# Kernel optimization log

Hardware: AMD Instinct MI355X
Metric: run time of the kernel (lower is better)

## Reference

```python
import jax, jax.numpy as jnp
import numpy as np

TAU_MEM = 20.0
TAU_SYN = 5.0
ALPHA_MEM = float(np.exp(-1.0 / TAU_MEM))
ALPHA_SYN = float(np.exp(-1.0 / TAU_SYN))
CONNECTIVITY = 0.1
SPECTRAL_RADIUS = 0.9


def setup_inputs() -> dict:
    key = jax.random.key(0)
    k1, k2, k3, k4 = jax.random.split(key, 4)
    B, D, N = 2048, 256, 512
    rates = jax.random.normal(k1, (B, D), dtype=jnp.float32)
    input_weight = jax.random.normal(k2, (N, D), dtype=jnp.float32) * 0.1
    W = jax.random.normal(k3, (N, N), dtype=jnp.float32)
    mask = (jax.random.uniform(k4, (N, N)) < CONNECTIVITY).astype(jnp.float32)
    W = W * mask
    # mirror torch init: scale by spectral_radius / max eigvalsh
    max_eig = jnp.linalg.eigvalsh(W)[-1]
    W = W * (SPECTRAL_RADIUS / max_eig)
    return {
        "rates": rates,
        "input_weight": input_weight,
        "reservoir_weight": W,
        "v_mem": jnp.zeros((B, N), dtype=jnp.float32),
        "current": jnp.zeros((B, N), dtype=jnp.float32),
        "n_steps": 64,
    }


def reference(rates, input_weight, reservoir_weight, v_mem, current, n_steps):
    dtype = rates.dtype
    # input current is identical every step in the original loop -> hoist it
    input_current = rates @ input_weight.T  # (B, N)

    def step(carry, _):
        v, c, spike_sum = carry
        rec = (c > 0).astype(dtype) @ reservoir_weight  # (B, N)
        c = ALPHA_SYN * c + (1.0 - ALPHA_SYN) * (input_current + rec)
        v = ALPHA_MEM * v + (1.0 - ALPHA_MEM) * c
        spike_sum = spike_sum + (v > 0).astype(dtype)
        return (v, c, spike_sum), None

    (v, c, spike_sum), _ = jax.lax.scan(
        step, (v_mem, current, jnp.zeros_like(v_mem)), None, length=n_steps
    )
    readout = spike_sum / n_steps  # == stack(spikes).mean(dim=1)
    return readout, (v, c)
```

## Files before the change

### kernel.cpp

```cpp
#include <hip/hip_runtime.h>
#include <stdint.h>


#define N_NEU 512
#define B_ROWS 2048
#define D_IN 256
#define R_PB 8
#define NBLK (B_ROWS / R_PB)

#define WS_PERM    0
#define WS_RANK    2048
#define WS_CNT     4096
#define WS_CNTW    8192
#define WS_IBASE   8256
#define WS_WBASE   8320
#define WS_IDX     16384
#define WS_WT      81920

#define SPK_OFF(k)  ((k) << 3)
#define SPK_BUF     4096

__global__ __launch_bounds__(256) void lsm_count(
    const float* __restrict__ W, uint32_t* __restrict__ ws)
{
    int t  = threadIdx.x;
    int k0 = blockIdx.x * 4;
    int c0 = 0, c1 = 0;
    #pragma unroll
    for (int kk = 0; kk < 4; ++kk) {
        const float* row = W + (size_t)(k0 + kk) * N_NEU;
        c0 += (row[t]       != 0.0f) ? 1 : 0;
        c1 += (row[t + 256] != 0.0f) ? 1 : 0;
    }
    if (c0) atomicAdd(&ws[(WS_CNT >> 2) + t],       (uint32_t)c0);
    if (c1) atomicAdd(&ws[(WS_CNT >> 2) + t + 256], (uint32_t)c1);
}

__global__ __launch_bounds__(512) void lsm_sort(uint32_t* __restrict__ ws)
{
    __shared__ int hist[N_NEU + 1];
    __shared__ int csort[N_NEU];
    __shared__ int gcw[8];

    int t = threadIdx.x;
    int creal = (int)ws[(WS_CNT >> 2) + t];
    for (int i = t; i < N_NEU + 1; i += 512) hist[i] = 0;
    __syncthreads();
    atomicAdd(&hist[creal], 1);
    __syncthreads();
    if (t == 0) {
        int acc = 0;
        for (int v = 0; v <= N_NEU; ++v) { int h = hist[v]; hist[v] = acc; acc += h; }
    }
    __syncthreads();
    int rank = atomicAdd(&hist[creal], 1);
    ws[(WS_PERM >> 2) + rank] = (uint32_t)t;
    ws[(WS_RANK >> 2) + t]    = (uint32_t)rank;
    csort[rank] = creal;
    __syncthreads();
    if (t < 8) {
        int cw = csort[t * 64 + 63];
        cw = (cw + 7) & ~7;
        gcw[t] = cw;
        ws[(WS_CNTW >> 2) + t] = (uint32_t)cw;
    }
    __syncthreads();
    if (t == 0) {
        int ai = 0, aw = 0;
        for (int g = 0; g < 8; ++g) {
            ws[(WS_IBASE >> 2) + g] = (uint32_t)ai;
            ws[(WS_WBASE >> 2) + g] = (uint32_t)aw;
            ai += gcw[g] * 64 * 2;
            aw += gcw[g] * 64 * 4;
        }
    }
    __syncthreads();
    int wg = rank >> 6, ls = rank & 63;
    int cw = gcw[wg];
    uint32_t ib = ws[(WS_IBASE >> 2) + wg];
    uint32_t wb = ws[(WS_WBASE >> 2) + wg];
    char* base = (char*)ws;
    for (int j = creal; j < cw; ++j) {
        *(unsigned short*)(base + WS_IDX + ib + (j >> 3) * 1024 + ls * 16 + (j & 7) * 2) = 0;
        *(float*)(base + WS_WT + wb + (j >> 3) * 2048 + ls * 32 + (j & 7) * 4) = 0.0f;
    }
}

__global__ __launch_bounds__(64) void lsm_fill(
    const float* __restrict__ W, uint32_t* __restrict__ ws)
{
    int c    = blockIdx.x;
    int lane = threadIdx.x;
    char* base = (char*)ws;
    uint32_t rank = ws[(WS_RANK >> 2) + c];
    int wg = (int)(rank >> 6), ls = (int)(rank & 63);
    uint32_t ib = ws[(WS_IBASE >> 2) + wg];
    uint32_t wb = ws[(WS_WBASE >> 2) + wg];

    __shared__ int ctr;
    if (lane == 0) ctr = 0;
    __syncthreads();

    for (int k = lane; k < N_NEU; k += 64) {
        float wv = W[(size_t)k * N_NEU + c];
        if (wv != 0.0f) {
            int j = atomicAdd(&ctr, 1);
            *(unsigned short*)(base + WS_IDX + ib + (j >> 3) * 1024 + ls * 16 + (j & 7) * 2)
                = (unsigned short)SPK_OFF(k);
            *(float*)(base + WS_WT + wb + (j >> 3) * 2048 + ls * 32 + (j & 7) * 4) = wv;
        }
    }
}

#define GATH(P, X, B) \
    P##0 = *(const uint2*)((B) + ((X).x & 0xffffu)); \
    P##1 = *(const uint2*)((B) + ((X).x >> 16));     \
    P##2 = *(const uint2*)((B) + ((X).y & 0xffffu)); \
    P##3 = *(const uint2*)((B) + ((X).y >> 16));     \
    P##4 = *(const uint2*)((B) + ((X).z & 0xffffu)); \
    P##5 = *(const uint2*)((B) + ((X).z >> 16));     \
    P##6 = *(const uint2*)((B) + ((X).w & 0xffffu)); \
    P##7 = *(const uint2*)((B) + ((X).w >> 16));

#define C1(S, W) \
    rec0 = fmaf((W), (float)((S).x & 0xffu),         rec0); \
    rec1 = fmaf((W), (float)(((S).x >> 8) & 0xffu),  rec1); \
    rec2 = fmaf((W), (float)(((S).x >> 16) & 0xffu), rec2); \
    rec3 = fmaf((W), (float)((S).x >> 24),           rec3); \
    rec4 = fmaf((W), (float)((S).y & 0xffu),         rec4); \
    rec5 = fmaf((W), (float)(((S).y >> 8) & 0xffu),  rec5); \
    rec6 = fmaf((W), (float)(((S).y >> 16) & 0xffu), rec6); \
    rec7 = fmaf((W), (float)((S).y >> 24),           rec7);

#define CONS(P, WA, WB) \
    C1(P##0, (WA).x) C1(P##1, (WA).y) C1(P##2, (WA).z) C1(P##3, (WA).w) \
    C1(P##4, (WB).x) C1(P##5, (WB).y) C1(P##6, (WB).z) C1(P##7, (WB).w)

#define LDW(WA, WB, K) \
    WA = ((const float4*)(wp0 + (K) * 2048))[0]; \
    WB = ((const float4*)(wp0 + (K) * 2048))[1];

__global__ __launch_bounds__(512, 1)
void lsm_main(
    const float* __restrict__ rates, const float* __restrict__ inW,
    const float* __restrict__ vin,   const float* __restrict__ cin,
    const int* __restrict__ nsteps_p,
    const uint32_t* __restrict__ ws, float* __restrict__ out)
{
    __shared__ __align__(16) unsigned char smem[2 * SPK_BUF + 16384];
    float* stg = (float*)(smem + 2 * SPK_BUF);
    float* rl  = stg;

    int q    = threadIdx.x;
    int blk  = blockIdx.x;
    int r0   = blk * R_PB;
    int w    = q >> 6;
    int lane = q & 63;
    int wg   = (w < 4) ? w : (11 - w);
    int n    = (int)ws[(WS_PERM >> 2) + wg * 64 + lane];
    int cw   = (int)ws[(WS_CNTW >> 2) + wg];
    int nit  = cw >> 3;
    const char* ip0 = (const char*)ws + WS_IDX + ws[(WS_IBASE >> 2) + wg]
                    + lane * 16;
    const char* wp0 = (const char*)ws + WS_WT  + ws[(WS_WBASE >> 2) + wg]
                    + lane * 32;
    int spk_n = SPK_OFF(n);

    float c0v[R_PB], v0v[R_PB];
    #pragma unroll
    for (int r = 0; r < R_PB; ++r)
        stg[r * N_NEU + q] = cin[(size_t)(r0 + r) * N_NEU + q];
    __syncthreads();
    #pragma unroll
    for (int r = 0; r < R_PB; ++r) c0v[r] = stg[r * N_NEU + n];
    __syncthreads();
    #pragma unroll
    for (int r = 0; r < R_PB; ++r)
        stg[r * N_NEU + q] = vin[(size_t)(r0 + r) * N_NEU + q];
    __syncthreads();
    #pragma unroll
    for (int r = 0; r < R_PB; ++r) v0v[r] = stg[r * N_NEU + n];
    __syncthreads();

    ((float4*)rl)[q] = ((const float4*)(rates + (size_t)r0 * D_IN))[q];
    __syncthreads();

    float I[R_PB] = {0.f, 0.f, 0.f, 0.f, 0.f, 0.f, 0.f, 0.f};
    {
        const float4* wrow = (const float4*)(inW + (size_t)n * D_IN);
        for (int d4 = 0; d4 < D_IN / 4; ++d4) {
            float4 wv = wrow[d4];
            #pragma unroll
            for (int r = 0; r < R_PB; ++r) {
                const float* rr = rl + r * D_IN + d4 * 4;
                I[r] += wv.x * rr[0] + wv.y * rr[1] + wv.z * rr[2] + wv.w * rr[3];
            }
        }
    }

    uint2 sini = make_uint2(0u, 0u);
    #pragma unroll
    for (int r = 0; r < R_PB; ++r) {
        unsigned bit = (c0v[r] > 0.f) ? 1u : 0u;
        if (r < 4) sini.x |= bit << (r * 8);
        else       sini.y |= bit << ((r - 4) * 8);
    }
    *(uint2*)(smem + spk_n) = sini;

    unsigned ssx = 0u, ssy = 0u;

    uint4 xr0, xr1, xr2, xr3, xr4, xr5, xr6, xr7, xr8, xr9, xr10, xr11;
    const uint4 xz = make_uint4(0u, 0u, 0u, 0u);
    xr0  =              *(const uint4*)(ip0);
    xr1  = (1  < nit) ? *(const uint4*)(ip0 + 1024)  : xz;
    xr2  = (2  < nit) ? *(const uint4*)(ip0 + 2048)  : xz;
    xr3  = (3  < nit) ? *(const uint4*)(ip0 + 3072)  : xz;
    xr4  = (4  < nit) ? *(const uint4*)(ip0 + 4096)  : xz;
    xr5  = (5  < nit) ? *(const uint4*)(ip0 + 5120)  : xz;
    xr6  = (6  < nit) ? *(const uint4*)(ip0 + 6144)  : xz;
    xr7  = (7  < nit) ? *(const uint4*)(ip0 + 7168)  : xz;
    xr8  = (8  < nit) ? *(const uint4*)(ip0 + 8192)  : xz;
    xr9  = (9  < nit) ? *(const uint4*)(ip0 + 9216)  : xz;
    xr10 = (10 < nit) ? *(const uint4*)(ip0 + 10240) : xz;
    xr11 = (11 < nit) ? *(const uint4*)(ip0 + 11264) : xz;

    float4 rw0a, rw0b, rw1a, rw1b, rw2a, rw2b;
    const float4 fz = make_float4(0.f, 0.f, 0.f, 0.f);
    rw0a = ((const float4*)wp0)[0];
    rw0b = ((const float4*)wp0)[1];
    rw1a = (1 < nit) ? ((const float4*)(wp0 + 2048))[0] : fz;
    rw1b = (1 < nit) ? ((const float4*)(wp0 + 2048))[1] : fz;
    rw2a = (2 < nit) ? ((const float4*)(wp0 + 4096))[0] : fz;
    rw2b = (2 < nit) ? ((const float4*)(wp0 + 4096))[1] : fz;

    const float AS   = (float)0.8187307530779818;
    const float OMAS = (float)(1.0 - 0.8187307530779818);
    const float AM   = (float)0.9512294245007140;
    const float OMAM = (float)(1.0 - 0.9512294245007140);

    int T = nsteps_p[0];
    __syncthreads();

    #pragma unroll 1
    for (int t = 0; t < T; ++t) {
        const unsigned char* sb = smem + ((t & 1) ? SPK_BUF : 0);
        unsigned char*       db = smem + ((t & 1) ? 0 : SPK_BUF);

        float rec0 = 0.f, rec1 = 0.f, rec2 = 0.f, rec3 = 0.f;
        float rec4 = 0.f, rec5 = 0.f, rec6 = 0.f, rec7 = 0.f;
        uint2 a0, a1, a2, a3, a4, a5, a6, a7;
        uint2 b0, b1, b2, b3, b4, b5, b6, b7;
        float4 waA, wbA, waB, wbB, waC, wbC;

        GATH(a, xr0, sb)
        if (3 < nit) { LDW(waA, wbA, 3) }
        if (4 < nit) { LDW(waB, wbB, 4) }
        if (1 < nit) { GATH(b, xr1, sb) }
        CONS(a, rw0a, rw0b)
        if (1 < nit) {
            if (2 < nit) { GATH(a, xr2, sb) }
            CONS(b, rw1a, rw1b)
        }
        if (2 < nit) {
            if (5 < nit) { LDW(waC, wbC, 5) }
            if (3 < nit) { GATH(b, xr3, sb) }
            CONS(a, rw2a, rw2b)
        }
        if (3 < nit) {
            if (4 < nit) { GATH(a, xr4, sb) }
            CONS(b, waA, wbA)
            if (6 < nit) { LDW(waA, wbA, 6) }
        }
        if (4 < nit) {
            if (5 < nit) { GATH(b, xr5, sb) }
            CONS(a, waB, wbB)
            if (7 < nit) { LDW(waB, wbB, 7) }
        }
        if (5 < nit) {
            if (6 < nit) { GATH(a, xr6, sb) }
            CONS(b, waC, wbC)
            if (8 < nit) { LDW(waC, wbC, 8) }
        }
        if (6 < nit) {
            if (7 < nit) { GATH(b, xr7, sb) }
            CONS(a, waA, wbA)
            if (9 < nit) { LDW(waA, wbA, 9) }
        }
        if (7 < nit) {
            if (8 < nit) { GATH(a, xr8, sb) }
            CONS(b, waB, wbB)
            if (10 < nit) { LDW(waB, wbB, 10) }
        }
        if (8 < nit) {
            if (9 < nit) { GATH(b, xr9, sb) }
            CONS(a, waC, wbC)
            if (11 < nit) { LDW(waC, wbC, 11) }
        }
        if (9 < nit) {
            if (10 < nit) { GATH(a, xr10, sb) }
            CONS(b, waA, wbA)
        }
        if (10 < nit) {
            if (11 < nit) { GATH(b, xr11, sb) }
            CONS(a, waB, wbB)
        }
        if (11 < nit) {
            CONS(b, waC, wbC)
        }

        uint2 ns = make_uint2(0u, 0u);
        unsigned vbx = 0u, vby = 0u;
        {
            float rca[R_PB] = {rec0, rec1, rec2, rec3, rec4, rec5, rec6, rec7};
            #pragma unroll
            for (int r = 0; r < R_PB; ++r) {
                c0v[r] = AS * c0v[r] + OMAS * (I[r] + rca[r]);
                v0v[r] = AM * v0v[r] + OMAM * c0v[r];
                unsigned cb = (c0v[r] > 0.f) ? 1u : 0u;
                unsigned vb = (v0v[r] > 0.f) ? 1u : 0u;
                if (r < 4) { ns.x |= cb << (r * 8);       vbx |= vb << (r * 8); }
                else       { ns.y |= cb << ((r - 4) * 8); vby |= vb << ((r - 4) * 8); }
            }
        }
        ssx += vbx;
        ssy += vby;
        *(uint2*)(db + spk_n) = ns;
        __syncthreads();
    }

    float invT = 1.0f / (float)T;
    size_t BN = (size_t)B_ROWS * N_NEU;

    #pragma unroll
    for (int r = 0; r < R_PB; ++r) {
        unsigned cnt = (r < 4) ? ((ssx >> (r * 8)) & 0xffu)
                               : ((ssy >> ((r - 4) * 8)) & 0xffu);
        stg[r * N_NEU + n] = (float)cnt * invT;
    }
    __syncthreads();
    #pragma unroll
    for (int r = 0; r < R_PB; ++r)
        out[(size_t)(r0 + r) * N_NEU + q] = stg[r * N_NEU + q];
    __syncthreads();

    #pragma unroll
    for (int r = 0; r < R_PB; ++r) stg[r * N_NEU + n] = v0v[r];
    __syncthreads();
    #pragma unroll
    for (int r = 0; r < R_PB; ++r)
        out[BN + (size_t)(r0 + r) * N_NEU + q] = stg[r * N_NEU + q];
    __syncthreads();

    #pragma unroll
    for (int r = 0; r < R_PB; ++r) stg[r * N_NEU + n] = c0v[r];
    __syncthreads();
    #pragma unroll
    for (int r = 0; r < R_PB; ++r)
        out[2 * BN + (size_t)(r0 + r) * N_NEU + q] = stg[r * N_NEU + q];
}

extern "C" void kernel_launch(void* const* d_in, const int* in_sizes, int n_in,
                              void* d_out, int out_size, void* d_ws, size_t ws_size,
                              hipStream_t stream)
{
    const float* rates = (const float*)d_in[0];
    const float* inW   = (const float*)d_in[1];
    const float* W     = (const float*)d_in[2];
    const float* vin   = (const float*)d_in[3];
    const float* cin   = (const float*)d_in[4];
    const int*   nst   = (const int*)d_in[5];
    uint32_t* ws = (uint32_t*)d_ws;
    float* out = (float*)d_out;
    (void)in_sizes; (void)n_in; (void)out_size; (void)ws_size;

    hipMemsetAsync((char*)d_ws + WS_CNT, 0, 2048, stream);

    lsm_count<<<128, 256, 0, stream>>>(W, ws);
    lsm_sort<<<1, 512, 0, stream>>>(ws);
    lsm_fill<<<N_NEU, 64, 0, stream>>>(W, ws);
    lsm_main<<<NBLK, 512, 0, stream>>>(rates, inW, vin, cin, nst, ws, out);
}
```

Baseline: 371.5 us.

## Store spikes as fp16 and accumulate with v_fma_mix to drop conversions

Spike flags in shared memory change from packed bytes to packed fp16 ones (0x3C00), doubling the spike buffer to 16 bytes per neuron. The inner accumulation uses inline v_fma_mix_f32 with op_sel to multiply fp32 weights by fp16 spike halves directly, removing the byte extract and int-to-float conversion per FMA. The weight prefetch schedule is also simplified to a two-slot double buffer loaded each step instead of preloaded registers plus a three-slot ring. In exchange, LDS gathers become 16-byte instead of 8-byte, doubling LDS traffic, and weights are reloaded from memory every step.

New measurement: 328.7 us. 1.13x faster.

```diff
diff --git a/kernel.cpp b/kernel.cpp
--- a/kernel.cpp
+++ b/kernel.cpp
@@ -17,8 +17,10 @@
 #define WS_IDX     16384
 #define WS_WT      81920
 
-#define SPK_OFF(k)  ((k) << 3)
-#define SPK_BUF     4096
+#define SPK_OFF(k)  ((k) << 4)
+#define SPK_BUF     8192
+
+#define H16_ONE 0x3C00u
 
 __global__ __launch_bounds__(256) void lsm_count(
     const float* __restrict__ W, uint32_t* __restrict__ ws)
@@ -113,24 +115,27 @@
 }
 
 #define GATH(P, X, B) \
-    P##0 = *(const uint2*)((B) + ((X).x & 0xffffu)); \
-    P##1 = *(const uint2*)((B) + ((X).x >> 16));     \
-    P##2 = *(const uint2*)((B) + ((X).y & 0xffffu)); \
-    P##3 = *(const uint2*)((B) + ((X).y >> 16));     \
-    P##4 = *(const uint2*)((B) + ((X).z & 0xffffu)); \
-    P##5 = *(const uint2*)((B) + ((X).z >> 16));     \
-    P##6 = *(const uint2*)((B) + ((X).w & 0xffffu)); \
-    P##7 = *(const uint2*)((B) + ((X).w >> 16));
-
-#define C1(S, W) \
-    rec0 = fmaf((W), (float)((S).x & 0xffu),         rec0); \
-    rec1 = fmaf((W), (float)(((S).x >> 8) & 0xffu),  rec1); \
-    rec2 = fmaf((W), (float)(((S).x >> 16) & 0xffu), rec2); \
-    rec3 = fmaf((W), (float)((S).x >> 24),           rec3); \
-    rec4 = fmaf((W), (float)((S).y & 0xffu),         rec4); \
-    rec5 = fmaf((W), (float)(((S).y >> 8) & 0xffu),  rec5); \
-    rec6 = fmaf((W), (float)(((S).y >> 16) & 0xffu), rec6); \
-    rec7 = fmaf((W), (float)((S).y >> 24),           rec7);
+    P##0 = *(const uint4*)((B) + ((X).x & 0xffffu)); \
+    P##1 = *(const uint4*)((B) + ((X).x >> 16));     \
+    P##2 = *(const uint4*)((B) + ((X).y & 0xffffu)); \
+    P##3 = *(const uint4*)((B) + ((X).y >> 16));     \
+    P##4 = *(const uint4*)((B) + ((X).z & 0xffffu)); \
+    P##5 = *(const uint4*)((B) + ((X).z >> 16));     \
+    P##6 = *(const uint4*)((B) + ((X).w & 0xffffu)); \
+    P##7 = *(const uint4*)((B) + ((X).w >> 16));
+
+#define FMIX_LO(ACC, WV, S) \
+    asm("v_fma_mix_f32 %0, %1, %2, %0 op_sel:[0,0,0] op_sel_hi:[0,1,0]" \
+        : "+v"(ACC) : "v"(WV), "v"(S));
+#define FMIX_HI(ACC, WV, S) \
+    asm("v_fma_mix_f32 %0, %1, %2, %0 op_sel:[0,1,0] op_sel_hi:[0,1,0]" \
+        : "+v"(ACC) : "v"(WV), "v"(S));
+
+#define C1(S, WV) \
+    FMIX_LO(rec0, WV, (S).x) FMIX_HI(rec1, WV, (S).x) \
+    FMIX_LO(rec2, WV, (S).y) FMIX_HI(rec3, WV, (S).y) \
+    FMIX_LO(rec4, WV, (S).z) FMIX_HI(rec5, WV, (S).z) \
+    FMIX_LO(rec6, WV, (S).w) FMIX_HI(rec7, WV, (S).w)
 
 #define CONS(P, WA, WB) \
     C1(P##0, (WA).x) C1(P##1, (WA).y) C1(P##2, (WA).z) C1(P##3, (WA).w) \
@@ -198,14 +203,17 @@
         }
     }
 
-    uint2 sini = make_uint2(0u, 0u);
+    uint4 sini = make_uint4(0u, 0u, 0u, 0u);
     #pragma unroll
     for (int r = 0; r < R_PB; ++r) {
-        unsigned bit = (c0v[r] > 0.f) ? 1u : 0u;
-        if (r < 4) sini.x |= bit << (r * 8);
-        else       sini.y |= bit << ((r - 4) * 8);
-    }
-    *(uint2*)(smem + spk_n) = sini;
+        unsigned hb = (c0v[r] > 0.f) ? H16_ONE : 0u;
+        unsigned sh = (r & 1) ? 16 : 0;
+        if (r < 2)      sini.x |= hb << sh;
+        else if (r < 4) sini.y |= hb << sh;
+        else if (r < 6) sini.z |= hb << sh;
+        else            sini.w |= hb << sh;
+    }
+    *(uint4*)(smem + spk_n) = sini;
 
     unsigned ssx = 0u, ssy = 0u;
 
@@ -224,15 +232,6 @@
     xr10 = (10 < nit) ? *(const uint4*)(ip0 + 10240) : xz;
     xr11 = (11 < nit) ? *(const uint4*)(ip0 + 11264) : xz;
 
-    float4 rw0a, rw0b, rw1a, rw1b, rw2a, rw2b;
-    const float4 fz = make_float4(0.f, 0.f, 0.f, 0.f);
-    rw0a = ((const float4*)wp0)[0];
-    rw0b = ((const float4*)wp0)[1];
-    rw1a = (1 < nit) ? ((const float4*)(wp0 + 2048))[0] : fz;
-    rw1b = (1 < nit) ? ((const float4*)(wp0 + 2048))[1] : fz;
-    rw2a = (2 < nit) ? ((const float4*)(wp0 + 4096))[0] : fz;
-    rw2b = (2 < nit) ? ((const float4*)(wp0 + 4096))[1] : fz;
-
     const float AS   = (float)0.8187307530779818;
     const float OMAS = (float)(1.0 - 0.8187307530779818);
     const float AM   = (float)0.9512294245007140;
@@ -248,67 +247,59 @@
 
         float rec0 = 0.f, rec1 = 0.f, rec2 = 0.f, rec3 = 0.f;
         float rec4 = 0.f, rec5 = 0.f, rec6 = 0.f, rec7 = 0.f;
-        uint2 a0, a1, a2, a3, a4, a5, a6, a7;
-        uint2 b0, b1, b2, b3, b4, b5, b6, b7;
-        float4 waA, wbA, waB, wbB, waC, wbC;
-
+        uint4 a0, a1, a2, a3, a4, a5, a6, a7;
+        uint4 b0, b1, b2, b3, b4, b5, b6, b7;
+        float4 waA, wbA, waB, wbB;
+
+        LDW(waA, wbA, 0)
         GATH(a, xr0, sb)
-        if (3 < nit) { LDW(waA, wbA, 3) }
-        if (4 < nit) { LDW(waB, wbB, 4) }
-        if (1 < nit) { GATH(b, xr1, sb) }
-        CONS(a, rw0a, rw0b)
-        if (1 < nit) {
-            if (2 < nit) { GATH(a, xr2, sb) }
-            CONS(b, rw1a, rw1b)
-        }
-        if (2 < nit) {
-            if (5 < nit) { LDW(waC, wbC, 5) }
-            if (3 < nit) { GATH(b, xr3, sb) }
-            CONS(a, rw2a, rw2b)
-        }
-        if (3 < nit) {
-            if (4 < nit) { GATH(a, xr4, sb) }
-            CONS(b, waA, wbA)
-            if (6 < nit) { LDW(waA, wbA, 6) }
-        }
-        if (4 < nit) {
-            if (5 < nit) { GATH(b, xr5, sb) }
-            CONS(a, waB, wbB)
-            if (7 < nit) { LDW(waB, wbB, 7) }
-        }
-        if (5 < nit) {
-            if (6 < nit) { GATH(a, xr6, sb) }
-            CONS(b, waC, wbC)
-            if (8 < nit) { LDW(waC, wbC, 8) }
-        }
-        if (6 < nit) {
-            if (7 < nit) { GATH(b, xr7, sb) }
-            CONS(a, waA, wbA)
-            if (9 < nit) { LDW(waA, wbA, 9) }
-        }
-        if (7 < nit) {
-            if (8 < nit) { GATH(a, xr8, sb) }
-            CONS(b, waB, wbB)
-            if (10 < nit) { LDW(waB, wbB, 10) }
-        }
-        if (8 < nit) {
-            if (9 < nit) { GATH(b, xr9, sb) }
-            CONS(a, waC, wbC)
-            if (11 < nit) { LDW(waC, wbC, 11) }
-        }
-        if (9 < nit) {
-            if (10 < nit) { GATH(a, xr10, sb) }
-            CONS(b, waA, wbA)
+        if (1 < nit)  { LDW(waB, wbB, 1)  GATH(b, xr1, sb)  }
+        CONS(a, waA, wbA)
+        if (1 < nit)  {
+            if (2 < nit)  { LDW(waA, wbA, 2)  GATH(a, xr2, sb)  }
+            CONS(b, waB, wbB)
+        }
+        if (2 < nit)  {
+            if (3 < nit)  { LDW(waB, wbB, 3)  GATH(b, xr3, sb)  }
+            CONS(a, waA, wbA)
+        }
+        if (3 < nit)  {
+            if (4 < nit)  { LDW(waA, wbA, 4)  GATH(a, xr4, sb)  }
+            CONS(b, waB, wbB)
+        }
+        if (4 < nit)  {
+            if (5 < nit)  { LDW(waB, wbB, 5)  GATH(b, xr5, sb)  }
+            CONS(a, waA, wbA)
+        }
+        if (5 < nit)  {
+            if (6 < nit)  { LDW(waA, wbA, 6)  GATH(a, xr6, sb)  }
+            CONS(b, waB, wbB)
+        }
+        if (6 < nit)  {
+            if (7 < nit)  { LDW(waB, wbB, 7)  GATH(b, xr7, sb)  }
+            CONS(a, waA, wbA)
+        }
+        if (7 < nit)  {
+            if (8 < nit)  { LDW(waA, wbA, 8)  GATH(a, xr8, sb)  }
+            CONS(b, waB, wbB)
+        }
+        if (8 < nit)  {
+            if (9 < nit)  { LDW(waB, wbB, 9)  GATH(b, xr9, sb)  }
+            CONS(a, waA, wbA)
+        }
+        if (9 < nit)  {
+            if (10 < nit) { LDW(waA, wbA, 10) GATH(a, xr10, sb) }
+            CONS(b, waB, wbB)
         }
         if (10 < nit) {
-            if (11 < nit) { GATH(b, xr11, sb) }
-            CONS(a, waB, wbB)
+            if (11 < nit) { LDW(waB, wbB, 11) GATH(b, xr11, sb) }
+            CONS(a, waA, wbA)
         }
         if (11 < nit) {
-            CONS(b, waC, wbC)
-        }
-
-        uint2 ns = make_uint2(0u, 0u);
+            CONS(b, waB, wbB)
+        }
+
+        uint4 ns = make_uint4(0u, 0u, 0u, 0u);
         unsigned vbx = 0u, vby = 0u;
         {
             float rca[R_PB] = {rec0, rec1, rec2, rec3, rec4, rec5, rec6, rec7};
@@ -316,15 +307,20 @@
             for (int r = 0; r < R_PB; ++r) {
                 c0v[r] = AS * c0v[r] + OMAS * (I[r] + rca[r]);
                 v0v[r] = AM * v0v[r] + OMAM * c0v[r];
-                unsigned cb = (c0v[r] > 0.f) ? 1u : 0u;
+                unsigned hb = (c0v[r] > 0.f) ? H16_ONE : 0u;
                 unsigned vb = (v0v[r] > 0.f) ? 1u : 0u;
-                if (r < 4) { ns.x |= cb << (r * 8);       vbx |= vb << (r * 8); }
-                else       { ns.y |= cb << ((r - 4) * 8); vby |= vb << ((r - 4) * 8); }
+                unsigned sh = (r & 1) ? 16 : 0;
+                if (r < 2)      ns.x |= hb << sh;
+                else if (r < 4) ns.y |= hb << sh;
+                else if (r < 6) ns.z |= hb << sh;
+                else            ns.w |= hb << sh;
+                if (r < 4) vbx |= vb << (r * 8);
+                else       vby |= vb << ((r - 4) * 8);
             }
         }
         ssx += vbx;
         ssy += vby;
-        *(uint2*)(db + spk_n) = ns;
+        *(uint4*)(db + spk_n) = ns;
         __syncthreads();
     }
 
```
